# Kernel tuning notes

Measured on AMD Instinct MI355X. Metric: run time of the kernel, lower is better.

## Reference

```python
import jax, jax.numpy as jnp
import numpy as np

N_NODES = 200000
N_EDGES = 1600000
NUM_GRAPHS = 2000
VOCAB = 10000
D = 64
NUM_CLS = 2


def setup_inputs() -> dict:
    key = jax.random.key(0)
    ks = jax.random.split(key, 12)
    x = jax.random.randint(ks[0], (N_NODES,), 0, VOCAB, dtype=jnp.int32)
    edge_index = jax.random.randint(ks[1], (2, N_EDGES), 0, N_NODES, dtype=jnp.int32)
    edge_type = jax.random.randint(ks[2], (N_EDGES,), 0, 8, dtype=jnp.int32)
    batch = jnp.sort(jax.random.randint(ks[3], (N_NODES,), 0, NUM_GRAPHS, dtype=jnp.int32))
    embed_table = jax.random.normal(ks[4], (VOCAB, D), dtype=jnp.float32) * 0.02
    embed_table = embed_table.at[0].set(0.0)  # padding_idx=0
    W1 = jax.random.normal(ks[5], (D, D), dtype=jnp.float32) * (1.0 / np.sqrt(D))
    b1 = jnp.zeros((D,), dtype=jnp.float32)
    W2 = jax.random.normal(ks[6], (D, D), dtype=jnp.float32) * (1.0 / np.sqrt(D))
    b2 = jnp.zeros((D,), dtype=jnp.float32)
    Wlin = jax.random.normal(ks[7], (D, NUM_CLS), dtype=jnp.float32) * (1.0 / np.sqrt(D))
    blin = jnp.zeros((NUM_CLS,), dtype=jnp.float32)
    return {"x": x, "edge_index": edge_index, "edge_type": edge_type, "batch": batch,
            "embed_table": embed_table, "W1": W1, "b1": b1, "W2": W2, "b2": b2,
            "Wlin": Wlin, "blin": blin}


def reference(x, edge_index, edge_type, batch, embed_table, W1, b1, W2, b2, Wlin, blin):
    n = x.shape[0]
    # GCN normalization with self-loops (PyG GCNConv default, edge weight = 1)
    loops = jnp.arange(n, dtype=edge_index.dtype)
    src = jnp.concatenate([edge_index[0], loops])
    dst = jnp.concatenate([edge_index[1], loops])
    deg = jax.ops.segment_sum(jnp.ones_like(src, dtype=jnp.float32), dst, num_segments=n)
    dinv = jax.lax.rsqrt(deg)  # deg >= 1 due to self-loops
    norm = (dinv[src] * dinv[dst])[:, None]  # [E+N, 1]

    def gcn(h, W, b):
        h = h @ W  # transform first (small GEMM)
        agg = jax.ops.segment_sum(norm * h[src], dst, num_segments=n)
        return agg + b

    h = embed_table[x]                      # [N, D] embedding lookup
    h = jax.nn.relu(gcn(h, W1, b1))
    h = jax.nn.relu(gcn(h, W2, b2))
    # global mean pool over graphs
    sums = jax.ops.segment_sum(h, batch, num_segments=NUM_GRAPHS)
    cnts = jax.ops.segment_sum(jnp.ones((n,), dtype=h.dtype), batch, num_segments=NUM_GRAPHS)
    g = sums / jnp.maximum(cnts, 1.0)[:, None]
    return g @ Wlin + blin
```

## Files before the change

kernel.cpp:

```cpp
#include <hip/hip_runtime.h>
#include <hip/hip_fp16.h>


#define DD 64
#define BKT 256
#define MAXK 1024
#define NBLK 256
#define SLACK 772

typedef _Float16 half8_t __attribute__((ext_vector_type(8)));
typedef float float4_t __attribute__((ext_vector_type(4)));
union F4H8 { float4 f; half8_t h; };
union H8   { float4 f; __half2 h[4]; };

static __device__ __forceinline__ void atomAddF(float* p, float v) {
    unsafeAtomicAdd(p, v);
}

__global__ __launch_bounds__(256) void bin_count_kernel(
        const int* __restrict__ dst, int E, int CH,
        int* __restrict__ hist, int K,
        const float2* __restrict__ table2, __half2* __restrict__ th2, int n2,
        const float* __restrict__ W1, const float* __restrict__ W2,
        __half* __restrict__ w1t, __half* __restrict__ w2t) {
    __shared__ int lh[MAXK];
    int tid = threadIdx.x;
    for (int i = tid; i < K; i += 256) lh[i] = 0;
    __syncthreads();
    int stride = gridDim.x * 256;
    for (int i = blockIdx.x * 256 + tid; i < n2; i += stride)
        th2[i] = __float22half2_rn(table2[i]);
    for (int i = blockIdx.x * 256 + tid; i < DD * DD; i += stride) {
        int n = i >> 6, k = i & 63;
        w1t[i] = __float2half(W1[k * DD + n]);
        w2t[i] = __float2half(W2[k * DD + n]);
    }
    int e0 = blockIdx.x * CH;
    int e1 = min(E, e0 + CH);
    for (int e = e0 + tid; e < e1; e += 256)
        atomicAdd(&lh[((unsigned)dst[e]) >> 8], 1);
    __syncthreads();
    for (int b = tid; b < K; b += 256)
        hist[blockIdx.x * MAXK + b] = lh[b];
}

__global__ __launch_bounds__(256) void totals_kernel(
        const int* __restrict__ hist, int* __restrict__ bts,
        float* __restrict__ outacc, int K, int G2) {
    int g0 = blockIdx.x * 256 + threadIdx.x;
    int stride = gridDim.x * 256;
    for (int i = g0; i < G2; i += stride) outacc[i] = 0.f;
    for (int b = g0; b < K; b += stride) {
        int s = 0;
        for (int blk = 0; blk < NBLK; ++blk) s += hist[blk * MAXK + b];
        bts[b] = s;
    }
}

__global__ __launch_bounds__(256) void scan_bb_kernel(
        const int* __restrict__ bts, int* __restrict__ bb, int K, int E) {
    __shared__ int part[256];
    int tid = threadIdx.x;
    int CH2 = (K + 255) / 256;
    int base = tid * CH2;
    int s = 0;
    for (int i = 0; i < CH2; ++i) {
        int idx = base + i;
        if (idx < K) s += bts[idx];
    }
    part[tid] = s;
    __syncthreads();
    if (tid < 64) {
        int carry = 0;
        for (int c = 0; c < 4; ++c) {
            int orig = part[c * 64 + tid];
            int v = orig;
            #pragma unroll
            for (int off = 1; off < 64; off <<= 1) {
                int t = __shfl_up(v, off);
                if (tid >= off) v += t;
            }
            int tot = __shfl(v, 63);
            part[c * 64 + tid] = v - orig + carry;
            carry += tot;
        }
    }
    __syncthreads();
    int run = part[tid];
    for (int i = 0; i < CH2; ++i) {
        int idx = base + i;
        if (idx < K) {
            bb[idx] = run;
            run += bts[idx];
        }
    }
    if (tid == 0) bb[K] = E;
}

__global__ __launch_bounds__(256) void scanB_kernel(
        const int* __restrict__ hist, const int* __restrict__ bb,
        int* __restrict__ cur, int K) {
    int wid = (blockIdx.x * 256 + threadIdx.x) >> 6;
    int lane = threadIdx.x & 63;
    if (wid >= K) return;
    int b = wid;
    int v0 = hist[(lane * 4 + 0) * MAXK + b];
    int v1 = hist[(lane * 4 + 1) * MAXK + b];
    int v2 = hist[(lane * 4 + 2) * MAXK + b];
    int v3 = hist[(lane * 4 + 3) * MAXK + b];
    int sum = v0 + v1 + v2 + v3;
    int pref = sum;
    #pragma unroll
    for (int off = 1; off < 64; off <<= 1) {
        int t = __shfl_up(pref, off);
        if (lane >= off) pref += t;
    }
    int run = bb[b] + pref - sum;
    cur[(lane * 4 + 0) * MAXK + b] = run; run += v0;
    cur[(lane * 4 + 1) * MAXK + b] = run; run += v1;
    cur[(lane * 4 + 2) * MAXK + b] = run; run += v2;
    cur[(lane * 4 + 3) * MAXK + b] = run;
}

__global__ __launch_bounds__(256) void fill_kernel(
        const int* __restrict__ src, const int* __restrict__ dst, int E, int CH,
        const int* __restrict__ cur, int* __restrict__ pairbuf, int K) {
    __shared__ int lcur[MAXK];
    int tid = threadIdx.x;
    for (int b = tid; b < K; b += 256)
        lcur[b] = cur[blockIdx.x * MAXK + b];
    __syncthreads();
    int e0 = blockIdx.x * CH;
    int e1 = min(E, e0 + CH);
    for (int e = e0 + tid; e < e1; e += 256) {
        int s = src[e], d = dst[e];
        int pos = atomicAdd(&lcur[((unsigned)d) >> 8], 1);
        pairbuf[pos] = s | ((d & 255) << 24);
    }
}

__global__ __launch_bounds__(256) void build_csr_kernel(
        const int* __restrict__ pairbuf, const int* __restrict__ bnd,
        const int* __restrict__ x, int2* __restrict__ rowinfo,
        float2* __restrict__ xd,
        int* __restrict__ csr_src, __half* __restrict__ g1h, int N) {
    __shared__ int cnt[256], basel[256], curl[256];
    int tid = threadIdx.x;
    int b = blockIdx.x;
    int node0 = b << 8;
    cnt[tid] = 0;
    __syncthreads();
    int bb0 = bnd[b], bb1 = bnd[b + 1];
    for (int i = bb0 + tid; i < bb1; i += 256)
        atomicAdd(&cnt[((unsigned)pairbuf[i]) >> 24], 1);
    __syncthreads();
    int c  = cnt[tid];
    int pc = (c + 3) & ~3;
    {
        __syncthreads();
        basel[tid] = pc;
        __syncthreads();
        if (tid < 64) {
            int carry = 0;
            for (int cc = 0; cc < 4; ++cc) {
                int orig = basel[cc * 64 + tid];
                int v = orig;
                #pragma unroll
                for (int off = 1; off < 64; off <<= 1) {
                    int t = __shfl_up(v, off);
                    if (tid >= off) v += t;
                }
                int tot = __shfl(v, 63);
                cnt[cc * 64 + tid] = v - orig + carry;
                carry += tot;
            }
        }
        __syncthreads();
    }
    int cb0 = ((bb0 + 3) & ~3) + SLACK * b;
    int node = node0 + tid;
    int myBase = cb0 + cnt[tid];
    curl[tid] = myBase;
    if (node < N) {
        rowinfo[node] = make_int2(myBase, pc);
        xd[node] = make_float2(rsqrtf((float)c + 1.0f), __int_as_float(x[node]));
        for (int t = c; t < pc; ++t) csr_src[myBase + t] = N;
    } else if (node == N) {
        xd[N] = make_float2(0.0f, __int_as_float(0));
        float2* z = (float2*)(g1h + (size_t)N * DD);
        for (int t = 0; t < DD / 4; ++t) z[t] = make_float2(0.f, 0.f);
    }
    __syncthreads();
    for (int i = bb0 + tid; i < bb1; i += 256) {
        int pk = pairbuf[i];
        int pos = atomicAdd(&curl[((unsigned)pk) >> 24], 1);
        csr_src[pos] = pk & 0x00FFFFFF;
    }
}

__global__ __launch_bounds__(256, 6) void layer1_kernel(
        const int2* __restrict__ rowinfo,
        const int* __restrict__ csr_src, const float2* __restrict__ xd,
        const float4* __restrict__ th4, const __half* __restrict__ wt,
        const float* __restrict__ bias, __half* __restrict__ g1h, int N) {
    __shared__ float4 Hs4[32 * 9];
    __shared__ float dvs[32];
    int row0 = blockIdx.x * 32;
    int tid = threadIdx.x;
    int node_l = tid >> 3, j3 = tid & 7;
    int node = row0 + node_l;
    H8 acc0, acc1, acc2, acc3;
    acc0.f = make_float4(0.f, 0.f, 0.f, 0.f);
    acc1.f = acc0.f; acc2.f = acc0.f; acc3.f = acc0.f;
    __half2 dh = __float2half2_rn(0.f);
    if (node < N) {
        float2 sxd = xd[node];
        float di = sxd.x;
        if (j3 == 0) dvs[node_l] = di;
        dh = __float2half2_rn(di);
        H8 tv; tv.f = th4[(size_t)__float_as_int(sxd.y) * 8 + j3];
        acc0.h[0] = __hmul2(dh, tv.h[0]); acc0.h[1] = __hmul2(dh, tv.h[1]);
        acc0.h[2] = __hmul2(dh, tv.h[2]); acc0.h[3] = __hmul2(dh, tv.h[3]);
        int2 ri = rowinfo[node];
        const int4* cs = (const int4*)(csr_src + ri.x);
        int nq = ri.y >> 2;
        int q = 0;
        for (; q + 1 < nq; q += 2) {
            int4 sA = cs[q], sB = cs[q + 1];
            float2 pa = xd[sA.x], pb = xd[sA.y], pc_ = xd[sA.z], pd = xd[sA.w];
            float2 pe = xd[sB.x], pf = xd[sB.y], pg = xd[sB.z], ph = xd[sB.w];
            H8 u0, u1, u2, u3, u4, u5, u6, u7;
            u0.f = th4[(size_t)__float_as_int(pa.y)  * 8 + j3];
            u1.f = th4[(size_t)__float_as_int(pb.y)  * 8 + j3];
            u2.f = th4[(size_t)__float_as_int(pc_.y) * 8 + j3];
            u3.f = th4[(size_t)__float_as_int(pd.y)  * 8 + j3];
            u4.f = th4[(size_t)__float_as_int(pe.y)  * 8 + j3];
            u5.f = th4[(size_t)__float_as_int(pf.y)  * 8 + j3];
            u6.f = th4[(size_t)__float_as_int(pg.y)  * 8 + j3];
            u7.f = th4[(size_t)__float_as_int(ph.y)  * 8 + j3];
            __half2 w0 = __float2half2_rn(pa.x), w1 = __float2half2_rn(pb.x);
            __half2 w2 = __float2half2_rn(pc_.x), w3 = __float2half2_rn(pd.x);
            __half2 w4 = __float2half2_rn(pe.x), w5 = __float2half2_rn(pf.x);
            __half2 w6 = __float2half2_rn(pg.x), w7 = __float2half2_rn(ph.x);
            #pragma unroll
            for (int t = 0; t < 4; ++t) {
                acc0.h[t] = __hfma2(w0, u0.h[t], acc0.h[t]);
                acc1.h[t] = __hfma2(w1, u1.h[t], acc1.h[t]);
                acc2.h[t] = __hfma2(w2, u2.h[t], acc2.h[t]);
                acc3.h[t] = __hfma2(w3, u3.h[t], acc3.h[t]);
                acc0.h[t] = __hfma2(w4, u4.h[t], acc0.h[t]);
                acc1.h[t] = __hfma2(w5, u5.h[t], acc1.h[t]);
                acc2.h[t] = __hfma2(w6, u6.h[t], acc2.h[t]);
                acc3.h[t] = __hfma2(w7, u7.h[t], acc3.h[t]);
            }
        }
        if (q < nq) {
            int4 sA = cs[q];
            float2 pa = xd[sA.x], pb = xd[sA.y], pc_ = xd[sA.z], pd = xd[sA.w];
            H8 u0, u1, u2, u3;
            u0.f = th4[(size_t)__float_as_int(pa.y)  * 8 + j3];
            u1.f = th4[(size_t)__float_as_int(pb.y)  * 8 + j3];
            u2.f = th4[(size_t)__float_as_int(pc_.y) * 8 + j3];
            u3.f = th4[(size_t)__float_as_int(pd.y)  * 8 + j3];
            __half2 w0 = __float2half2_rn(pa.x), w1 = __float2half2_rn(pb.x);
            __half2 w2 = __float2half2_rn(pc_.x), w3 = __float2half2_rn(pd.x);
            #pragma unroll
            for (int t = 0; t < 4; ++t) {
                acc0.h[t] = __hfma2(w0, u0.h[t], acc0.h[t]);
                acc1.h[t] = __hfma2(w1, u1.h[t], acc1.h[t]);
                acc2.h[t] = __hfma2(w2, u2.h[t], acc2.h[t]);
                acc3.h[t] = __hfma2(w3, u3.h[t], acc3.h[t]);
            }
        }
        #pragma unroll
        for (int t = 0; t < 4; ++t)
            acc0.h[t] = __hmul2(dh, __hadd2(__hadd2(acc0.h[t], acc1.h[t]),
                                            __hadd2(acc2.h[t], acc3.h[t])));
    }
    Hs4[node_l * 9 + j3] = acc0.f;
    __syncthreads();

    int wave = tid >> 6, lane = tid & 63;
    int m = lane & 15, quad = lane >> 4;
    int ncol = wave * 16 + m;
    F4H8 b0, b1;
    const float4* WT4 = (const float4*)wt;
    b0.f = WT4[ncol * 8 + quad];
    b1.f = WT4[ncol * 8 + 4 + quad];
    float bb_ = bias[ncol];
    #pragma unroll
    for (int t = 0; t < 2; ++t) {
        F4H8 a0, a1;
        a0.f = Hs4[(t * 16 + m) * 9 + quad];
        a1.f = Hs4[(t * 16 + m) * 9 + 4 + quad];
        float4_t acc = {0.f, 0.f, 0.f, 0.f};
        acc = __builtin_amdgcn_mfma_f32_16x16x32_f16(a0.h, b0.h, acc, 0, 0, 0);
        acc = __builtin_amdgcn_mfma_f32_16x16x32_f16(a1.h, b1.h, acc, 0, 0, 0);
        #pragma unroll
        for (int reg = 0; reg < 4; ++reg) {
            int row = t * 16 + quad * 4 + reg;
            int grow = row0 + row;
            if (grow < N) {
                float h = fmaxf(acc[reg] + bb_, 0.0f);
                g1h[(size_t)grow * DD + ncol] = __float2half(dvs[row] * h);
            }
        }
    }
}

__global__ __launch_bounds__(256, 6) void layer2_pool_kernel(
        const int2* __restrict__ rowinfo,
        const int* __restrict__ csr_src, const float2* __restrict__ xd,
        const float4* __restrict__ g1h4, const __half* __restrict__ wt,
        const float* __restrict__ bias, const int* __restrict__ batch,
        const float* __restrict__ Wlin, float* __restrict__ outacc, int N) {
    __shared__ float4 Hs4[32 * 9];
    __shared__ float lp0[128], lp1[128];
    __shared__ float p0s[32], p1s[32];
    __shared__ int   bat[32];
    int row0 = blockIdx.x * 32;
    int tid = threadIdx.x;
    int node_l = tid >> 3, j3 = tid & 7;
    int node = row0 + node_l;
    H8 acc0, acc1, acc2, acc3;
    acc0.f = make_float4(0.f, 0.f, 0.f, 0.f);
    acc1.f = acc0.f; acc2.f = acc0.f; acc3.f = acc0.f;
    if (node < N) {
        float di = xd[node].x;
        acc0.f = g1h4[(size_t)node * 8 + j3];
        int2 ri = rowinfo[node];
        const int4* cs = (const int4*)(csr_src + ri.x);
        int nq = ri.y >> 2;
        int q = 0;
        for (; q + 1 < nq; q += 2) {
            int4 sA = cs[q], sB = cs[q + 1];
            H8 u0, u1, u2, u3, u4, u5, u6, u7;
            u0.f = g1h4[(size_t)sA.x * 8 + j3];
            u1.f = g1h4[(size_t)sA.y * 8 + j3];
            u2.f = g1h4[(size_t)sA.z * 8 + j3];
            u3.f = g1h4[(size_t)sA.w * 8 + j3];
            u4.f = g1h4[(size_t)sB.x * 8 + j3];
            u5.f = g1h4[(size_t)sB.y * 8 + j3];
            u6.f = g1h4[(size_t)sB.z * 8 + j3];
            u7.f = g1h4[(size_t)sB.w * 8 + j3];
            #pragma unroll
            for (int t = 0; t < 4; ++t) {
                acc0.h[t] = __hadd2(acc0.h[t], u0.h[t]);
                acc1.h[t] = __hadd2(acc1.h[t], u1.h[t]);
                acc2.h[t] = __hadd2(acc2.h[t], u2.h[t]);
                acc3.h[t] = __hadd2(acc3.h[t], u3.h[t]);
                acc0.h[t] = __hadd2(acc0.h[t], u4.h[t]);
                acc1.h[t] = __hadd2(acc1.h[t], u5.h[t]);
                acc2.h[t] = __hadd2(acc2.h[t], u6.h[t]);
                acc3.h[t] = __hadd2(acc3.h[t], u7.h[t]);
            }
        }
        if (q < nq) {
            int4 sA = cs[q];
            H8 u0, u1, u2, u3;
            u0.f = g1h4[(size_t)sA.x * 8 + j3];
            u1.f = g1h4[(size_t)sA.y * 8 + j3];
            u2.f = g1h4[(size_t)sA.z * 8 + j3];
            u3.f = g1h4[(size_t)sA.w * 8 + j3];
            #pragma unroll
            for (int t = 0; t < 4; ++t) {
                acc0.h[t] = __hadd2(acc0.h[t], u0.h[t]);
                acc1.h[t] = __hadd2(acc1.h[t], u1.h[t]);
                acc2.h[t] = __hadd2(acc2.h[t], u2.h[t]);
                acc3.h[t] = __hadd2(acc3.h[t], u3.h[t]);
            }
        }
        __half2 dih = __float2half2_rn(di);
        #pragma unroll
        for (int t = 0; t < 4; ++t)
            acc0.h[t] = __hmul2(dih, __hadd2(__hadd2(acc0.h[t], acc1.h[t]),
                                             __hadd2(acc2.h[t], acc3.h[t])));
    }
    Hs4[node_l * 9 + j3] = acc0.f;
    __syncthreads();

    int wave = tid >> 6, lane = tid & 63;
    int m = lane & 15, quad = lane >> 4;
    int ncol = wave * 16 + m;
    F4H8 b0, b1;
    const float4* WT4 = (const float4*)wt;
    b0.f = WT4[ncol * 8 + quad];
    b1.f = WT4[ncol * 8 + 4 + quad];
    float bb_  = bias[ncol];
    float wl0 = Wlin[ncol * 2 + 0];
    float wl1 = Wlin[ncol * 2 + 1];
    #pragma unroll
    for (int t = 0; t < 2; ++t) {
        F4H8 a0, a1;
        a0.f = Hs4[(t * 16 + m) * 9 + quad];
        a1.f = Hs4[(t * 16 + m) * 9 + 4 + quad];
        float4_t acc = {0.f, 0.f, 0.f, 0.f};
        acc = __builtin_amdgcn_mfma_f32_16x16x32_f16(a0.h, b0.h, acc, 0, 0, 0);
        acc = __builtin_amdgcn_mfma_f32_16x16x32_f16(a1.h, b1.h, acc, 0, 0, 0);
        #pragma unroll
        for (int reg = 0; reg < 4; ++reg) {
            int row = t * 16 + quad * 4 + reg;
            int grow = row0 + row;
            float h = (grow < N) ? fmaxf(acc[reg] + bb_, 0.0f) : 0.0f;
            float p0 = h * wl0;
            float p1 = h * wl1;
            #pragma unroll
            for (int off = 8; off >= 1; off >>= 1) {
                p0 += __shfl_xor(p0, off);
                p1 += __shfl_xor(p1, off);
            }
            if (m == 0) {
                lp0[wave * 32 + row] = p0;
                lp1[wave * 32 + row] = p1;
            }
        }
    }
    __syncthreads();
    if (tid < 32) {
        int grow = row0 + tid;
        p0s[tid] = lp0[tid] + lp0[32 + tid] + lp0[64 + tid] + lp0[96 + tid];
        p1s[tid] = lp1[tid] + lp1[32 + tid] + lp1[64 + tid] + lp1[96 + tid];
        bat[tid] = (grow < N) ? batch[grow] : -1;
    }
    __syncthreads();
    if (tid < 32) {
        int bg = bat[tid];
        bool head = (bg >= 0) && (tid == 0 || bat[tid - 1] != bg);
        if (head) {
            float s0 = 0.f, s1 = 0.f;
            for (int k = tid; k < 32 && bat[k] == bg; ++k) {
                s0 += p0s[k];
                s1 += p1s[k];
            }
            atomAddF(&outacc[bg * 2 + 0], s0);
            atomAddF(&outacc[bg * 2 + 1], s1);
        }
    }
}

__global__ void final_kernel(const float* __restrict__ outacc,
                             const int* __restrict__ batch,
                             const float* __restrict__ blin,
                             float* __restrict__ out, int G, int N) {
    int t = blockIdx.x * blockDim.x + threadIdx.x;
    if (t >= G * 2) return;
    int g = t >> 1, c = t & 1;
    int lo = 0, hi = N;
    while (lo < hi) { int m = (lo + hi) >> 1; if (batch[m] < g) lo = m + 1; else hi = m; }
    int lo2 = lo, hi2 = N;
    while (lo2 < hi2) { int m = (lo2 + hi2) >> 1; if (batch[m] < g + 1) lo2 = m + 1; else hi2 = m; }
    float cnt = (float)(lo2 - lo);
    out[t] = outacc[t] / fmaxf(cnt, 1.0f) + blin[c];
}

extern "C" void kernel_launch(void* const* d_in, const int* in_sizes, int n_in,
                              void* d_out, int out_size, void* d_ws, size_t ws_size,
                              hipStream_t stream) {
    const int*   x      = (const int*)d_in[0];
    const int*   ei     = (const int*)d_in[1];
    const int*   batch  = (const int*)d_in[3];
    const float* table  = (const float*)d_in[4];
    const float* W1     = (const float*)d_in[5];
    const float* b1     = (const float*)d_in[6];
    const float* W2     = (const float*)d_in[7];
    const float* b2     = (const float*)d_in[8];
    const float* Wlin   = (const float*)d_in[9];
    const float* blin   = (const float*)d_in[10];
    float* out = (float*)d_out;

    const int N = in_sizes[0];
    const int E = in_sizes[2];
    const int G = out_size / 2;
    const int TBL = in_sizes[4];

    const int* src = ei;
    const int* dst = ei + E;

    const int K = (N + BKT - 1) / BKT;
    const int M = NBLK * MAXK;
    const int CH = (E + NBLK - 1) / NBLK;
    const int CSRSZ = E + SLACK * K + 64;

    __half* g1h     = (__half*)d_ws;
    __half* th      = g1h + (size_t)(N + 1) * DD;
    __half* w1t     = th + TBL;
    __half* w2t     = w1t + DD * DD;
    int*    pairbuf = (int*)(w2t + DD * DD);
    int*    csr_src = pairbuf + E;
    int2*   rowinfo = (int2*)(csr_src + CSRSZ);
    float2* xd      = (float2*)(rowinfo + N);
    float*  outacc  = (float*)(xd + N + 1);
    int*    bb      = (int*)(outacc + 2 * G);
    int*    bts     = bb + K + 1;
    int*    hist    = bts + K;
    int*    cur     = hist + M;

    const int BT = 256;

    bin_count_kernel<<<NBLK, BT, 0, stream>>>(dst, E, CH, hist, K,
                                              (const float2*)table,
                                              (__half2*)th, TBL / 2,
                                              W1, W2, w1t, w2t);
    totals_kernel<<<16, BT, 0, stream>>>(hist, bts, outacc, K, 2 * G);
    scan_bb_kernel<<<1, BT, 0, stream>>>(bts, bb, K, E);
    scanB_kernel<<<(K * 64 + BT - 1) / BT, BT, 0, stream>>>(hist, bb, cur, K);
    fill_kernel<<<NBLK, BT, 0, stream>>>(src, dst, E, CH, cur, pairbuf, K);
    build_csr_kernel<<<K, BT, 0, stream>>>(pairbuf, bb, x, rowinfo, xd,
                                           csr_src, g1h, N);

    int gRow = (N + 31) / 32;
    layer1_kernel<<<gRow, BT, 0, stream>>>(rowinfo, csr_src, xd,
                                           (const float4*)th, w1t, b1, g1h, N);
    layer2_pool_kernel<<<gRow, BT, 0, stream>>>(rowinfo, csr_src, xd,
                                                (const float4*)g1h, w2t, b2,
                                                batch, Wlin, outacc, N);
    final_kernel<<<(G * 2 + BT - 1) / BT, BT, 0, stream>>>(outacc, batch, blin,
                                                           out, G, N);
}
```

Before: 240.2 us.

## Precompute dinv-scaled node embeddings, raise binning block count and occupancy

```diff
diff --git a/kernel.cpp b/kernel.cpp
--- a/kernel.cpp
+++ b/kernel.cpp
@@ -5,7 +5,7 @@
 #define DD 64
 #define BKT 256
 #define MAXK 1024
-#define NBLK 256
+#define NBLK 1024
 #define SLACK 772
 
 typedef _Float16 half8_t __attribute__((ext_vector_type(8)));
@@ -104,11 +104,14 @@
     int lane = threadIdx.x & 63;
     if (wid >= K) return;
     int b = wid;
-    int v0 = hist[(lane * 4 + 0) * MAXK + b];
-    int v1 = hist[(lane * 4 + 1) * MAXK + b];
-    int v2 = hist[(lane * 4 + 2) * MAXK + b];
-    int v3 = hist[(lane * 4 + 3) * MAXK + b];
-    int sum = v0 + v1 + v2 + v3;
+    const int PER = NBLK / 64;
+    int v[PER];
+    int sum = 0;
+    #pragma unroll
+    for (int i = 0; i < PER; ++i) {
+        v[i] = hist[(lane * PER + i) * MAXK + b];
+        sum += v[i];
+    }
     int pref = sum;
     #pragma unroll
     for (int off = 1; off < 64; off <<= 1) {
@@ -116,10 +119,11 @@
         if (lane >= off) pref += t;
     }
     int run = bb[b] + pref - sum;
-    cur[(lane * 4 + 0) * MAXK + b] = run; run += v0;
-    cur[(lane * 4 + 1) * MAXK + b] = run; run += v1;
-    cur[(lane * 4 + 2) * MAXK + b] = run; run += v2;
-    cur[(lane * 4 + 3) * MAXK + b] = run;
+    #pragma unroll
+    for (int i = 0; i < PER; ++i) {
+        cur[(lane * PER + i) * MAXK + b] = run;
+        run += v[i];
+    }
 }
 
 __global__ __launch_bounds__(256) void fill_kernel(
@@ -142,9 +146,12 @@
 __global__ __launch_bounds__(256) void build_csr_kernel(
         const int* __restrict__ pairbuf, const int* __restrict__ bnd,
         const int* __restrict__ x, int2* __restrict__ rowinfo,
-        float2* __restrict__ xd,
-        int* __restrict__ csr_src, __half* __restrict__ g1h, int N) {
+        float2* __restrict__ xd, const float4* __restrict__ th4,
+        int* __restrict__ csr_src, __half* __restrict__ g0h,
+        __half* __restrict__ g1h, int N) {
     __shared__ int cnt[256], basel[256], curl[256];
+    __shared__ float ldinv[256];
+    __shared__ int   lxi[256];
     int tid = threadIdx.x;
     int b = blockIdx.x;
     int node0 = b << 8;
@@ -181,14 +188,24 @@
     int node = node0 + tid;
     int myBase = cb0 + cnt[tid];
     curl[tid] = myBase;
+    ldinv[tid] = 0.f;
+    lxi[tid] = 0;
     if (node < N) {
+        float di = rsqrtf((float)c + 1.0f);
+        int xi = x[node];
         rowinfo[node] = make_int2(myBase, pc);
-        xd[node] = make_float2(rsqrtf((float)c + 1.0f), __int_as_float(x[node]));
+        xd[node] = make_float2(di, __int_as_float(xi));
+        ldinv[tid] = di;
+        lxi[tid] = xi;
         for (int t = c; t < pc; ++t) csr_src[myBase + t] = N;
     } else if (node == N) {
         xd[N] = make_float2(0.0f, __int_as_float(0));
-        float2* z = (float2*)(g1h + (size_t)N * DD);
-        for (int t = 0; t < DD / 4; ++t) z[t] = make_float2(0.f, 0.f);
+        float2* z1 = (float2*)(g1h + (size_t)N * DD);
+        float2* z0 = (float2*)(g0h + (size_t)N * DD);
+        for (int t = 0; t < DD / 4; ++t) {
+            z1[t] = make_float2(0.f, 0.f);
+            z0[t] = make_float2(0.f, 0.f);
+        }
     }
     __syncthreads();
     for (int i = bb0 + tid; i < bb1; i += 256) {
@@ -196,12 +213,24 @@
         int pos = atomicAdd(&curl[((unsigned)pk) >> 24], 1);
         csr_src[pos] = pk & 0x00FFFFFF;
     }
-}
-
-__global__ __launch_bounds__(256, 6) void layer1_kernel(
+    float4* g0h4 = (float4*)g0h;
+    for (int idx = tid; idx < 256 * 8; idx += 256) {
+        int n = idx >> 3, ch = idx & 7;
+        int gn = node0 + n;
+        if (gn < N) {
+            H8 tv; tv.f = th4[(size_t)lxi[n] * 8 + ch];
+            __half2 dh = __float2half2_rn(ldinv[n]);
+            #pragma unroll
+            for (int t = 0; t < 4; ++t) tv.h[t] = __hmul2(dh, tv.h[t]);
+            g0h4[(size_t)gn * 8 + ch] = tv.f;
+        }
+    }
+}
+
+__global__ __launch_bounds__(256, 8) void layer1_kernel(
         const int2* __restrict__ rowinfo,
         const int* __restrict__ csr_src, const float2* __restrict__ xd,
-        const float4* __restrict__ th4, const __half* __restrict__ wt,
+        const float4* __restrict__ g0h4, const __half* __restrict__ wt,
         const float* __restrict__ bias, __half* __restrict__ g1h, int N) {
     __shared__ float4 Hs4[32 * 9];
     __shared__ float dvs[32];
@@ -212,70 +241,57 @@
     H8 acc0, acc1, acc2, acc3;
     acc0.f = make_float4(0.f, 0.f, 0.f, 0.f);
     acc1.f = acc0.f; acc2.f = acc0.f; acc3.f = acc0.f;
-    __half2 dh = __float2half2_rn(0.f);
     if (node < N) {
-        float2 sxd = xd[node];
-        float di = sxd.x;
+        float di = xd[node].x;
         if (j3 == 0) dvs[node_l] = di;
-        dh = __float2half2_rn(di);
-        H8 tv; tv.f = th4[(size_t)__float_as_int(sxd.y) * 8 + j3];
-        acc0.h[0] = __hmul2(dh, tv.h[0]); acc0.h[1] = __hmul2(dh, tv.h[1]);
-        acc0.h[2] = __hmul2(dh, tv.h[2]); acc0.h[3] = __hmul2(dh, tv.h[3]);
+        acc0.f = g0h4[(size_t)node * 8 + j3];
         int2 ri = rowinfo[node];
         const int4* cs = (const int4*)(csr_src + ri.x);
         int nq = ri.y >> 2;
         int q = 0;
         for (; q + 1 < nq; q += 2) {
             int4 sA = cs[q], sB = cs[q + 1];
-            float2 pa = xd[sA.x], pb = xd[sA.y], pc_ = xd[sA.z], pd = xd[sA.w];
-            float2 pe = xd[sB.x], pf = xd[sB.y], pg = xd[sB.z], ph = xd[sB.w];
             H8 u0, u1, u2, u3, u4, u5, u6, u7;
-            u0.f = th4[(size_t)__float_as_int(pa.y)  * 8 + j3];
-            u1.f = th4[(size_t)__float_as_int(pb.y)  * 8 + j3];
-            u2.f = th4[(size_t)__float_as_int(pc_.y) * 8 + j3];
-            u3.f = th4[(size_t)__float_as_int(pd.y)  * 8 + j3];
-            u4.f = th4[(size_t)__float_as_int(pe.y)  * 8 + j3];
-            u5.f = th4[(size_t)__float_as_int(pf.y)  * 8 + j3];
-            u6.f = th4[(size_t)__float_as_int(pg.y)  * 8 + j3];
-            u7.f = th4[(size_t)__float_as_int(ph.y)  * 8 + j3];
-            __half2 w0 = __float2half2_rn(pa.x), w1 = __float2half2_rn(pb.x);
-            __half2 w2 = __float2half2_rn(pc_.x), w3 = __float2half2_rn(pd.x);
-            __half2 w4 = __float2half2_rn(pe.x), w5 = __float2half2_rn(pf.x);
-            __half2 w6 = __float2half2_rn(pg.x), w7 = __float2half2_rn(ph.x);
+            u0.f = g0h4[(size_t)sA.x * 8 + j3];
+            u1.f = g0h4[(size_t)sA.y * 8 + j3];
+            u2.f = g0h4[(size_t)sA.z * 8 + j3];
+            u3.f = g0h4[(size_t)sA.w * 8 + j3];
+            u4.f = g0h4[(size_t)sB.x * 8 + j3];
+            u5.f = g0h4[(size_t)sB.y * 8 + j3];
+            u6.f = g0h4[(size_t)sB.z * 8 + j3];
+            u7.f = g0h4[(size_t)sB.w * 8 + j3];
             #pragma unroll
             for (int t = 0; t < 4; ++t) {
-                acc0.h[t] = __hfma2(w0, u0.h[t], acc0.h[t]);
-                acc1.h[t] = __hfma2(w1, u1.h[t], acc1.h[t]);
-                acc2.h[t] = __hfma2(w2, u2.h[t], acc2.h[t]);
-                acc3.h[t] = __hfma2(w3, u3.h[t], acc3.h[t]);
-                acc0.h[t] = __hfma2(w4, u4.h[t], acc0.h[t]);
-                acc1.h[t] = __hfma2(w5, u5.h[t], acc1.h[t]);
-                acc2.h[t] = __hfma2(w6, u6.h[t], acc2.h[t]);
-                acc3.h[t] = __hfma2(w7, u7.h[t], acc3.h[t]);
+                acc0.h[t] = __hadd2(acc0.h[t], u0.h[t]);
+                acc1.h[t] = __hadd2(acc1.h[t], u1.h[t]);
+                acc2.h[t] = __hadd2(acc2.h[t], u2.h[t]);
+                acc3.h[t] = __hadd2(acc3.h[t], u3.h[t]);
+                acc0.h[t] = __hadd2(acc0.h[t], u4.h[t]);
+                acc1.h[t] = __hadd2(acc1.h[t], u5.h[t]);
+                acc2.h[t] = __hadd2(acc2.h[t], u6.h[t]);
+                acc3.h[t] = __hadd2(acc3.h[t], u7.h[t]);
             }
         }
         if (q < nq) {
             int4 sA = cs[q];
-            float2 pa = xd[sA.x], pb = xd[sA.y], pc_ = xd[sA.z], pd = xd[sA.w];
             H8 u0, u1, u2, u3;
-            u0.f = th4[(size_t)__float_as_int(pa.y)  * 8 + j3];
-            u1.f = th4[(size_t)__float_as_int(pb.y)  * 8 + j3];
-            u2.f = th4[(size_t)__float_as_int(pc_.y) * 8 + j3];
-            u3.f = th4[(size_t)__float_as_int(pd.y)  * 8 + j3];
-            __half2 w0 = __float2half2_rn(pa.x), w1 = __float2half2_rn(pb.x);
-            __half2 w2 = __float2half2_rn(pc_.x), w3 = __float2half2_rn(pd.x);
+            u0.f = g0h4[(size_t)sA.x * 8 + j3];
+            u1.f = g0h4[(size_t)sA.y * 8 + j3];
+            u2.f = g0h4[(size_t)sA.z * 8 + j3];
+            u3.f = g0h4[(size_t)sA.w * 8 + j3];
             #pragma unroll
             for (int t = 0; t < 4; ++t) {
-                acc0.h[t] = __hfma2(w0, u0.h[t], acc0.h[t]);
-                acc1.h[t] = __hfma2(w1, u1.h[t], acc1.h[t]);
-                acc2.h[t] = __hfma2(w2, u2.h[t], acc2.h[t]);
-                acc3.h[t] = __hfma2(w3, u3.h[t], acc3.h[t]);
-            }
-        }
+                acc0.h[t] = __hadd2(acc0.h[t], u0.h[t]);
+                acc1.h[t] = __hadd2(acc1.h[t], u1.h[t]);
+                acc2.h[t] = __hadd2(acc2.h[t], u2.h[t]);
+                acc3.h[t] = __hadd2(acc3.h[t], u3.h[t]);
+            }
+        }
+        __half2 dih = __float2half2_rn(di);
         #pragma unroll
         for (int t = 0; t < 4; ++t)
-            acc0.h[t] = __hmul2(dh, __hadd2(__hadd2(acc0.h[t], acc1.h[t]),
-                                            __hadd2(acc2.h[t], acc3.h[t])));
+            acc0.h[t] = __hmul2(dih, __hadd2(__hadd2(acc0.h[t], acc1.h[t]),
+                                             __hadd2(acc2.h[t], acc3.h[t])));
     }
     Hs4[node_l * 9 + j3] = acc0.f;
     __syncthreads();
@@ -308,7 +324,7 @@
     }
 }
 
-__global__ __launch_bounds__(256, 6) void layer2_pool_kernel(
+__global__ __launch_bounds__(256, 8) void layer2_pool_kernel(
         const int2* __restrict__ rowinfo,
         const int* __restrict__ csr_src, const float2* __restrict__ xd,
         const float4* __restrict__ g1h4, const __half* __restrict__ wt,
@@ -481,7 +497,8 @@
     const int CH = (E + NBLK - 1) / NBLK;
     const int CSRSZ = E + SLACK * K + 64;
 
-    __half* g1h     = (__half*)d_ws;
+    __half* g0h     = (__half*)d_ws;
+    __half* g1h     = g0h + (size_t)(N + 1) * DD;
     __half* th      = g1h + (size_t)(N + 1) * DD;
     __half* w1t     = th + TBL;
     __half* w2t     = w1t + DD * DD;
@@ -506,11 +523,12 @@
     scanB_kernel<<<(K * 64 + BT - 1) / BT, BT, 0, stream>>>(hist, bb, cur, K);
     fill_kernel<<<NBLK, BT, 0, stream>>>(src, dst, E, CH, cur, pairbuf, K);
     build_csr_kernel<<<K, BT, 0, stream>>>(pairbuf, bb, x, rowinfo, xd,
-                                           csr_src, g1h, N);
+                                           (const float4*)th, csr_src,
+                                           g0h, g1h, N);
 
     int gRow = (N + 31) / 32;
     layer1_kernel<<<gRow, BT, 0, stream>>>(rowinfo, csr_src, xd,
-                                           (const float4*)th, w1t, b1, g1h, N);
+                                           (const float4*)g0h, w1t, b1, g1h, N);
     layer2_pool_kernel<<<gRow, BT, 0, stream>>>(rowinfo, csr_src, xd,
                                                 (const float4*)g1h, w2t, b2,
                                                 batch, Wlin, outacc, N);
```

Measured after the change: 278.1 us. 15.8% more time.
